# Optimization experiments

Hardware: AMD Instinct MI355X
Metric: run time of the kernel (lower is better)

## Reference

```python
import jax, jax.numpy as jnp
import numpy as np

D_MODEL = 2048
NUM_HEADS = 32
NUM_GROUPS = 8
HEAD_DIM = D_MODEL // NUM_HEADS  # 64
HEADS_PER_GROUP = NUM_HEADS // NUM_GROUPS  # 4


def setup_inputs() -> dict:
    key = jax.random.key(0)
    ks = jax.random.split(key, 5)
    B, S = 1, 2048
    x = jax.random.normal(ks[0], (B, S, D_MODEL), dtype=jnp.float32)
    scale = 1.0 / np.sqrt(D_MODEL)
    w_q = jax.random.normal(ks[1], (D_MODEL, D_MODEL), dtype=jnp.float32) * scale
    w_k = jax.random.normal(ks[2], (D_MODEL, NUM_GROUPS * HEAD_DIM), dtype=jnp.float32) * scale
    w_v = jax.random.normal(ks[3], (D_MODEL, NUM_GROUPS * HEAD_DIM), dtype=jnp.float32) * scale
    w_o = jax.random.normal(ks[4], (D_MODEL, D_MODEL), dtype=jnp.float32) * scale
    return {"x": x, "w_q": w_q, "w_k": w_k, "w_v": w_v, "w_o": w_o}


def reference(x, w_q, w_k, w_v, w_o):
    B, S, _ = x.shape
    # projections (nn.Linear, no bias)
    q = (x @ w_q).reshape(B, S, NUM_HEADS, HEAD_DIM)          # [B,S,H,d]
    k = (x @ w_k).reshape(B, S, NUM_GROUPS, HEAD_DIM)         # [B,S,G,d]
    v = (x @ w_v).reshape(B, S, NUM_GROUPS, HEAD_DIM)
    # group queries: [B,S,G,hpg,d] so each KV group serves heads_per_group query heads
    qg = q.reshape(B, S, NUM_GROUPS, HEADS_PER_GROUP, HEAD_DIM)
    scale = 1.0 / jnp.sqrt(jnp.asarray(HEAD_DIM, dtype=x.dtype))
    # scores: [B,G,hpg,S_q,S_k] without duplicating K/V
    scores = jnp.einsum("bsghd,btgd->bghst", qg, k) * scale
    attn = jax.nn.softmax(scores, axis=-1)
    out = jnp.einsum("bghst,btgd->bsghd", attn, v)            # [B,S,G,hpg,d]
    out = out.reshape(B, S, D_MODEL)
    return out @ w_o
```

## Files before the change

kernel.cpp:

```cpp
#include <hip/hip_runtime.h>

typedef unsigned short ushort_t;
typedef __attribute__((ext_vector_type(8))) short short8;
typedef __attribute__((ext_vector_type(4))) float floatx4;

__device__ __forceinline__ unsigned short f2bf(float f) {
  unsigned int u = __float_as_uint(f);
  u += 0x7fffu + ((u >> 16) & 1u);
  return (unsigned short)(u >> 16);
}

__device__ __forceinline__ unsigned int cvt_pk_bf16(float a, float b) {
  unsigned int r;
  asm("v_cvt_pk_bf16_f32 %0, %1, %2" : "=v"(r) : "v"(a), "v"(b));
  return r;
}

__device__ __forceinline__ void gl_lds16(const void* g, void* l) {
  __builtin_amdgcn_global_load_lds((const __attribute__((address_space(1))) void*)g,
                                   (__attribute__((address_space(3))) void*)l,
                                   16, 0, 0);
}


__global__ void conv_x_kernel(const float* __restrict__ src, ushort_t* __restrict__ dst, int n4) {
  int i = blockIdx.x * blockDim.x + threadIdx.x;
  if (i >= n4) return;
  float4 v = ((const float4*)src)[i];
  union { ushort_t u[4]; unsigned long long ll; } o;
  o.u[0] = f2bf(v.x); o.u[1] = f2bf(v.y); o.u[2] = f2bf(v.z); o.u[3] = f2bf(v.w);
  ((unsigned long long*)dst)[i] = o.ll;
}

__global__ void transpose_conv(const float* __restrict__ src, ushort_t* __restrict__ dst,
                               int R, int C) {
  __shared__ float tile[32][33];
  int c0 = blockIdx.x * 32, r0 = blockIdx.y * 32;
  int tx = threadIdx.x, ty = threadIdx.y;
#pragma unroll
  for (int i = ty; i < 32; i += 8)
    tile[i][tx] = src[(long)(r0 + i) * C + c0 + tx];
  __syncthreads();
#pragma unroll
  for (int i = ty; i < 32; i += 8)
    dst[(long)(c0 + i) * R + r0 + tx] = f2bf(tile[tx][i]);
}

template <int EPI>
__global__ __launch_bounds__(256, 3) void gemm_bt(
    const ushort_t* __restrict__ A, const ushort_t* __restrict__ B,
    float* __restrict__ C,
    ushort_t* __restrict__ qb, ushort_t* __restrict__ kb, ushort_t* __restrict__ vb,
    int M, int N, int K) {
  __shared__ __attribute__((aligned(16))) ushort_t As[2][128 * 32];
  __shared__ __attribute__((aligned(16))) ushort_t Bs[2][128 * 32];
  const int t = threadIdx.x;
  const int w = t >> 6, lane = t & 63;
  const int m = lane & 15, quad = lane >> 4;
  const int nwg = gridDim.x * gridDim.y;
  const int bid = blockIdx.y * gridDim.x + blockIdx.x;
  const int sw = (bid & 7) * (nwg >> 3) + (bid >> 3);
  const int m0 = (sw / gridDim.x) * 128, n0 = (sw % gridDim.x) * 128;
  const int wr = w >> 1, wc = w & 1;

  floatx4 acc[4][4] = {};

  auto stage = [&](int kk, int buf) {
#pragma unroll
    for (int i = 0; i < 2; ++i) {
      int c = i * 256 + t;
      int c0 = i * 256 + w * 64;
      gl_lds16(A + (long)(m0 + (c >> 2)) * K + kk + (c & 3) * 8, As[buf] + c0 * 8);
      gl_lds16(B + (long)(n0 + (c >> 2)) * K + kk + (c & 3) * 8, Bs[buf] + c0 * 8);
    }
  };

  stage(0, 0);
  __syncthreads();
  int cur = 0;
  for (int kk = 0; kk < K; kk += 32) {
    if (kk + 32 < K) stage(kk + 32, cur ^ 1);
    short8 af[4], bf[4];
#pragma unroll
    for (int i = 0; i < 4; ++i)
      af[i] = *(const short8*)(As[cur] + (wr * 64 + i * 16 + m) * 32 + quad * 8);
#pragma unroll
    for (int j = 0; j < 4; ++j)
      bf[j] = *(const short8*)(Bs[cur] + (wc * 64 + j * 16 + m) * 32 + quad * 8);
#pragma unroll
    for (int i = 0; i < 4; ++i)
#pragma unroll
      for (int j = 0; j < 4; ++j)
        acc[i][j] = __builtin_amdgcn_mfma_f32_16x16x32_bf16(af[i], bf[j], acc[i][j], 0, 0, 0);
    __syncthreads();
    cur ^= 1;
  }

#pragma unroll
  for (int i = 0; i < 4; ++i)
#pragma unroll
    for (int j = 0; j < 4; ++j)
#pragma unroll
      for (int r = 0; r < 4; ++r) {
        float v = acc[i][j][r];
        int row = m0 + wr * 64 + i * 16 + quad * 4 + r;
        int col = n0 + wc * 64 + j * 16 + m;
        if (EPI == 1) {
          C[(long)row * N + col] = v;
        } else {
          if (col < 2048) {
            qb[((((col >> 6) * 2048) + row) << 6) | (col & 63)] = f2bf(v * 0.18033688f);
          } else if (col < 2560) {
            int g = (col - 2048) >> 6;
            kb[(((g * 2048) + row) << 6) | (col & 63)] = f2bf(v);
          } else {
            int g = (col - 2560) >> 6;
            vb[(long)((g << 6) | (col & 63)) * 2048 + row] = f2bf(v);
          }
        }
      }
}

__global__ __launch_bounds__(256, 4) void flash_kernel(
    const ushort_t* __restrict__ Q, const ushort_t* __restrict__ Kb,
    const ushort_t* __restrict__ Vb, ushort_t* __restrict__ O, int S) {
  __shared__ __attribute__((aligned(16))) ushort_t Ks[2][64 * 64];
  __shared__ __attribute__((aligned(16))) ushort_t Vs[2][64 * 64];
  __shared__ __attribute__((aligned(16))) ushort_t Ps[4 * 32 * 32];
  const int t = threadIdx.x;
  const int w = t >> 6, lane = t & 63;
  const int m = lane & 15, quad = lane >> 4;
  const int nwg = gridDim.x * gridDim.y;
  const int bid = blockIdx.y * gridDim.x + blockIdx.x;
  const int sw = (bid & 7) * (nwg >> 3) + (bid >> 3);
  const int h = sw / gridDim.x, g = h >> 2;
  const int q0 = (sw % gridDim.x) * 128;
  const ushort_t* qp = Q + (long)h * S * 64;
  const ushort_t* kp = Kb + (long)g * S * 64;
  const ushort_t* vp = Vb + (long)g * 64 * S;

  auto stage = [&](int t0, int buf) {
#pragma unroll
    for (int i = 0; i < 2; ++i) {
      int c = i * 256 + t;
      int c0 = i * 256 + w * 64;
      int sl = ((c & 3) ^ ((c >> 3) & 3)) * 8;
      gl_lds16(kp + (long)(t0 + ((c >> 2) & 63)) * 64 + (c >> 8) * 32 + sl, Ks[buf] + c0 * 8);
      gl_lds16(vp + (long)((c >> 2) & 63) * S + t0 + (c >> 8) * 32 + sl, Vs[buf] + c0 * 8);
    }
  };

  stage(0, 0);

  short8 qf[2][2];
#pragma unroll
  for (int rt = 0; rt < 2; ++rt)
#pragma unroll
    for (int kq = 0; kq < 2; ++kq)
      qf[rt][kq] = *(const short8*)(qp + (long)(q0 + w * 32 + rt * 16 + m) * 64 + kq * 32 + quad * 8);

  short8 ones;
#pragma unroll
  for (int z = 0; z < 8; ++z) ones[z] = (short)0x3F80;

  floatx4 lacc[2] = {};
  floatx4 oacc[2][4] = {};
  char* PwB = (char*)Ps + w * 2048;
  const int psw = (m & 3) << 4;
  const int kvswz = (quad ^ ((m >> 1) & 3)) * 8;

  __syncthreads();
  int cur = 0;
  for (int t0 = 0; t0 < S; t0 += 64) {
    if (t0 + 64 < S) stage(t0 + 64, cur ^ 1);

    floatx4 sacc[2][4] = {};
    __builtin_amdgcn_s_setprio(1);
#pragma unroll
    for (int ct = 0; ct < 4; ++ct) {
      short8 kf0 = *(const short8*)(Ks[cur] + (ct * 16 + m) * 32 + kvswz);
      short8 kf1 = *(const short8*)(Ks[cur] + 2048 + (ct * 16 + m) * 32 + kvswz);
#pragma unroll
      for (int rt = 0; rt < 2; ++rt) {
        sacc[rt][ct] = __builtin_amdgcn_mfma_f32_16x16x32_bf16(kf0, qf[rt][0], sacc[rt][ct], 0, 0, 0);
        sacc[rt][ct] = __builtin_amdgcn_mfma_f32_16x16x32_bf16(kf1, qf[rt][1], sacc[rt][ct], 0, 0, 0);
      }
    }
    __builtin_amdgcn_s_setprio(0);

#pragma unroll
    for (int hh = 0; hh < 2; ++hh) {
#pragma unroll
      for (int rt = 0; rt < 2; ++rt)
#pragma unroll
        for (int cl = 0; cl < 2; ++cl) {
          int ct = hh * 2 + cl;
          float p0 = exp2f(sacc[rt][ct][0]);
          float p1 = exp2f(sacc[rt][ct][1]);
          float p2 = exp2f(sacc[rt][ct][2]);
          float p3 = exp2f(sacc[rt][ct][3]);
          uint2 pk;
          pk.x = cvt_pk_bf16(p0, p1);
          pk.y = cvt_pk_bf16(p2, p3);
          *(uint2*)(PwB + rt * 1024 + m * 64 + ((cl * 32 + quad * 8) ^ psw)) = pk;
        }
      __builtin_amdgcn_s_setprio(1);
      short8 pf[2];
#pragma unroll
      for (int rt = 0; rt < 2; ++rt) {
        pf[rt] = *(const short8*)(PwB + rt * 1024 + m * 64 + ((quad * 16) ^ psw));
        lacc[rt] = __builtin_amdgcn_mfma_f32_16x16x32_bf16(pf[rt], ones, lacc[rt], 0, 0, 0);
      }
#pragma unroll
      for (int ct = 0; ct < 4; ++ct) {
        short8 vf = *(const short8*)(Vs[cur] + hh * 2048 + (ct * 16 + m) * 32 + kvswz);
#pragma unroll
        for (int rt = 0; rt < 2; ++rt)
          oacc[rt][ct] = __builtin_amdgcn_mfma_f32_16x16x32_bf16(pf[rt], vf, oacc[rt][ct], 0, 0, 0);
      }
      __builtin_amdgcn_s_setprio(0);
    }

    __syncthreads();
    cur ^= 1;
  }

#pragma unroll
  for (int rt = 0; rt < 2; ++rt)
#pragma unroll
    for (int r = 0; r < 4; ++r) {
      float inv = 1.f / lacc[rt][r];
      int srow = q0 + w * 32 + rt * 16 + quad * 4 + r;
#pragma unroll
      for (int ct = 0; ct < 4; ++ct)
        O[(long)srow * 2048 + h * 64 + ct * 16 + m] = f2bf(oacc[rt][ct][r] * inv);
    }
}


extern "C" void kernel_launch(void* const* d_in, const int* in_sizes, int n_in,
                              void* d_out, int out_size, void* d_ws, size_t ws_size,
                              hipStream_t stream) {
  (void)in_sizes; (void)n_in; (void)out_size; (void)ws_size;
  const float* x  = (const float*)d_in[0];
  const float* wq = (const float*)d_in[1];
  const float* wk = (const float*)d_in[2];
  const float* wv = (const float*)d_in[3];
  const float* wo = (const float*)d_in[4];
  float* out = (float*)d_out;
  char* ws = (char*)d_ws;
  const size_t MB = 1u << 20;

  ushort_t* xb    = (ushort_t*)(ws);
  ushort_t* wqkvT = (ushort_t*)(ws + 8 * MB);
  ushort_t* woT   = (ushort_t*)(ws + 20 * MB);
  ushort_t* qbuf  = (ushort_t*)(ws + 28 * MB);
  ushort_t* kbuf  = (ushort_t*)(ws + 36 * MB);
  ushort_t* vbuf  = (ushort_t*)(ws + 38 * MB);
  ushort_t* attn  = xb;

  conv_x_kernel<<<4096, 256, 0, stream>>>(x, xb, 2048 * 2048 / 4);
  dim3 tb(32, 8);
  transpose_conv<<<dim3(64, 64), tb, 0, stream>>>(wq, wqkvT, 2048, 2048);
  transpose_conv<<<dim3(16, 64), tb, 0, stream>>>(wk, wqkvT + 2048 * 2048, 2048, 512);
  transpose_conv<<<dim3(16, 64), tb, 0, stream>>>(wv, wqkvT + 2560 * 2048, 2048, 512);
  transpose_conv<<<dim3(64, 64), tb, 0, stream>>>(wo, woT, 2048, 2048);

  gemm_bt<0><<<dim3(24, 16), 256, 0, stream>>>(xb, wqkvT, nullptr, qbuf, kbuf, vbuf,
                                               2048, 3072, 2048);
  flash_kernel<<<dim3(16, 32), 256, 0, stream>>>(qbuf, kbuf, vbuf, attn, 2048);
  gemm_bt<1><<<dim3(16, 16), 256, 0, stream>>>(attn, woT, out, nullptr, nullptr, nullptr,
                                               2048, 2048, 2048);
}
```

Measured before the change: 274.5 us.

## Halve flash attention query tile to 64 rows and double grid size

Each workgroup of the flash kernel now handles 64 query rows (16 per wave) instead of 128, and the grid doubles to 1024 blocks. The P buffer layout changes to 16x64 per wave with a wider XOR swizzle, and the PV product runs over two 32-key halves at once. The aim is more parallelism across CUs and less register pressure per wave, so occupancy goes up. The cost is twice as many K/V tile loads from global memory per head, and each K/V fragment read from LDS is reused for fewer MFMAs.

```diff
diff --git a/kernel.cpp b/kernel.cpp
--- a/kernel.cpp
+++ b/kernel.cpp
@@ -126,7 +126,7 @@
     const ushort_t* __restrict__ Vb, ushort_t* __restrict__ O, int S) {
   __shared__ __attribute__((aligned(16))) ushort_t Ks[2][64 * 64];
   __shared__ __attribute__((aligned(16))) ushort_t Vs[2][64 * 64];
-  __shared__ __attribute__((aligned(16))) ushort_t Ps[4 * 32 * 32];
+  __shared__ __attribute__((aligned(16))) ushort_t Ps[4 * 16 * 64];
   const int t = threadIdx.x;
   const int w = t >> 6, lane = t & 63;
   const int m = lane & 15, quad = lane >> 4;
@@ -134,7 +134,7 @@
   const int bid = blockIdx.y * gridDim.x + blockIdx.x;
   const int sw = (bid & 7) * (nwg >> 3) + (bid >> 3);
   const int h = sw / gridDim.x, g = h >> 2;
-  const int q0 = (sw % gridDim.x) * 128;
+  const int q0 = (sw % gridDim.x) * 64;
   const ushort_t* qp = Q + (long)h * S * 64;
   const ushort_t* kp = Kb + (long)g * S * 64;
   const ushort_t* vp = Vb + (long)g * 64 * S;
@@ -152,21 +152,19 @@
 
   stage(0, 0);
 
-  short8 qf[2][2];
-#pragma unroll
-  for (int rt = 0; rt < 2; ++rt)
-#pragma unroll
-    for (int kq = 0; kq < 2; ++kq)
-      qf[rt][kq] = *(const short8*)(qp + (long)(q0 + w * 32 + rt * 16 + m) * 64 + kq * 32 + quad * 8);
+  short8 qf[2];
+#pragma unroll
+  for (int kq = 0; kq < 2; ++kq)
+    qf[kq] = *(const short8*)(qp + (long)(q0 + w * 16 + m) * 64 + kq * 32 + quad * 8);
 
   short8 ones;
 #pragma unroll
   for (int z = 0; z < 8; ++z) ones[z] = (short)0x3F80;
 
-  floatx4 lacc[2] = {};
-  floatx4 oacc[2][4] = {};
+  floatx4 lacc = {};
+  floatx4 oacc[4] = {};
   char* PwB = (char*)Ps + w * 2048;
-  const int psw = (m & 3) << 4;
+  const int psw = (m & 7) << 4;
   const int kvswz = (quad ^ ((m >> 1) & 3)) * 8;
 
   __syncthreads();
@@ -174,67 +172,54 @@
   for (int t0 = 0; t0 < S; t0 += 64) {
     if (t0 + 64 < S) stage(t0 + 64, cur ^ 1);
 
-    floatx4 sacc[2][4] = {};
+    floatx4 sacc[4] = {};
     __builtin_amdgcn_s_setprio(1);
 #pragma unroll
     for (int ct = 0; ct < 4; ++ct) {
       short8 kf0 = *(const short8*)(Ks[cur] + (ct * 16 + m) * 32 + kvswz);
       short8 kf1 = *(const short8*)(Ks[cur] + 2048 + (ct * 16 + m) * 32 + kvswz);
-#pragma unroll
-      for (int rt = 0; rt < 2; ++rt) {
-        sacc[rt][ct] = __builtin_amdgcn_mfma_f32_16x16x32_bf16(kf0, qf[rt][0], sacc[rt][ct], 0, 0, 0);
-        sacc[rt][ct] = __builtin_amdgcn_mfma_f32_16x16x32_bf16(kf1, qf[rt][1], sacc[rt][ct], 0, 0, 0);
+      sacc[ct] = __builtin_amdgcn_mfma_f32_16x16x32_bf16(kf0, qf[0], sacc[ct], 0, 0, 0);
+      sacc[ct] = __builtin_amdgcn_mfma_f32_16x16x32_bf16(kf1, qf[1], sacc[ct], 0, 0, 0);
+    }
+    __builtin_amdgcn_s_setprio(0);
+
+#pragma unroll
+    for (int ct = 0; ct < 4; ++ct) {
+      float p0 = exp2f(sacc[ct][0]);
+      float p1 = exp2f(sacc[ct][1]);
+      float p2 = exp2f(sacc[ct][2]);
+      float p3 = exp2f(sacc[ct][3]);
+      uint2 pk;
+      pk.x = cvt_pk_bf16(p0, p1);
+      pk.y = cvt_pk_bf16(p2, p3);
+      *(uint2*)(PwB + m * 128 + ((ct * 32 + quad * 8) ^ psw)) = pk;
+    }
+
+    __builtin_amdgcn_s_setprio(1);
+#pragma unroll
+    for (int kt = 0; kt < 2; ++kt) {
+      short8 pf = *(const short8*)(PwB + m * 128 + ((kt * 64 + quad * 16) ^ psw));
+      lacc = __builtin_amdgcn_mfma_f32_16x16x32_bf16(pf, ones, lacc, 0, 0, 0);
+#pragma unroll
+      for (int ct = 0; ct < 4; ++ct) {
+        short8 vf = *(const short8*)(Vs[cur] + kt * 2048 + (ct * 16 + m) * 32 + kvswz);
+        oacc[ct] = __builtin_amdgcn_mfma_f32_16x16x32_bf16(pf, vf, oacc[ct], 0, 0, 0);
       }
     }
     __builtin_amdgcn_s_setprio(0);
-
-#pragma unroll
-    for (int hh = 0; hh < 2; ++hh) {
-#pragma unroll
-      for (int rt = 0; rt < 2; ++rt)
-#pragma unroll
-        for (int cl = 0; cl < 2; ++cl) {
-          int ct = hh * 2 + cl;
-          float p0 = exp2f(sacc[rt][ct][0]);
-          float p1 = exp2f(sacc[rt][ct][1]);
-          float p2 = exp2f(sacc[rt][ct][2]);
-          float p3 = exp2f(sacc[rt][ct][3]);
-          uint2 pk;
-          pk.x = cvt_pk_bf16(p0, p1);
-          pk.y = cvt_pk_bf16(p2, p3);
-          *(uint2*)(PwB + rt * 1024 + m * 64 + ((cl * 32 + quad * 8) ^ psw)) = pk;
-        }
-      __builtin_amdgcn_s_setprio(1);
-      short8 pf[2];
-#pragma unroll
-      for (int rt = 0; rt < 2; ++rt) {
-        pf[rt] = *(const short8*)(PwB + rt * 1024 + m * 64 + ((quad * 16) ^ psw));
-        lacc[rt] = __builtin_amdgcn_mfma_f32_16x16x32_bf16(pf[rt], ones, lacc[rt], 0, 0, 0);
-      }
-#pragma unroll
-      for (int ct = 0; ct < 4; ++ct) {
-        short8 vf = *(const short8*)(Vs[cur] + hh * 2048 + (ct * 16 + m) * 32 + kvswz);
-#pragma unroll
-        for (int rt = 0; rt < 2; ++rt)
-          oacc[rt][ct] = __builtin_amdgcn_mfma_f32_16x16x32_bf16(pf[rt], vf, oacc[rt][ct], 0, 0, 0);
-      }
-      __builtin_amdgcn_s_setprio(0);
-    }
 
     __syncthreads();
     cur ^= 1;
   }
 
 #pragma unroll
-  for (int rt = 0; rt < 2; ++rt)
-#pragma unroll
-    for (int r = 0; r < 4; ++r) {
-      float inv = 1.f / lacc[rt][r];
-      int srow = q0 + w * 32 + rt * 16 + quad * 4 + r;
-#pragma unroll
-      for (int ct = 0; ct < 4; ++ct)
-        O[(long)srow * 2048 + h * 64 + ct * 16 + m] = f2bf(oacc[rt][ct][r] * inv);
-    }
+  for (int r = 0; r < 4; ++r) {
+    float inv = 1.f / lacc[r];
+    int srow = q0 + w * 16 + quad * 4 + r;
+#pragma unroll
+    for (int ct = 0; ct < 4; ++ct)
+      O[(long)srow * 2048 + h * 64 + ct * 16 + m] = f2bf(oacc[ct][r] * inv);
+  }
 }
 
 
@@ -268,7 +253,7 @@
 
   gemm_bt<0><<<dim3(24, 16), 256, 0, stream>>>(xb, wqkvT, nullptr, qbuf, kbuf, vbuf,
                                                2048, 3072, 2048);
-  flash_kernel<<<dim3(16, 32), 256, 0, stream>>>(qbuf, kbuf, vbuf, attn, 2048);
+  flash_kernel<<<dim3(32, 32), 256, 0, stream>>>(qbuf, kbuf, vbuf, attn, 2048);
   gemm_bt<1><<<dim3(16, 16), 256, 0, stream>>>(attn, woT, out, nullptr, nullptr, nullptr,
                                                2048, 2048, 2048);
 }
```

Result: faster. 263.8 us (-3.9%).
